# Kernel optimization log

Measured on AMD Instinct MI355X. Metric: run time of the kernel, lower is better.

The kernel has to match this reference:

```python
import jax, jax.numpy as jnp
import numpy as np

N = 50000      # nodes
E = 800000     # edges
D = 64         # out_feats
L = 5          # n_steps


def setup_inputs() -> dict:
    key = jax.random.key(0)
    ks = jax.random.split(key, 6)
    x = jax.random.normal(ks[0], (N, D), dtype=jnp.float32)
    edge_index = jax.random.randint(ks[1], (2, E), 0, N, dtype=jnp.int64)
    # per-layer message transform weights, uniform(-1/sqrt(D), 1/sqrt(D)) like PyG `uniform`
    bound = 1.0 / np.sqrt(D)
    weight = jax.random.uniform(ks[2], (L, D, D), minval=-bound, maxval=bound, dtype=jnp.float32)
    # GRUCell params (PyTorch layout: [3*D, D] with gate order r, z, n)
    w_ih = jax.random.uniform(ks[3], (3 * D, D), minval=-bound, maxval=bound, dtype=jnp.float32)
    w_hh = jax.random.uniform(ks[4], (3 * D, D), minval=-bound, maxval=bound, dtype=jnp.float32)
    b = jax.random.uniform(ks[5], (2, 3 * D), minval=-bound, maxval=bound, dtype=jnp.float32)
    return {"x": x, "edge_index": edge_index, "weight": weight,
            "w_ih": w_ih, "w_hh": w_hh, "b_ih": b[0], "b_hh": b[1]}


def _gru_cell(m, h, w_ih, w_hh, b_ih, b_hh):
    # PyTorch GRUCell semantics; gate order r, z, n
    gi = m @ w_ih.T + b_ih          # [N, 3D]
    gh = h @ w_hh.T + b_hh          # [N, 3D]
    i_r, i_z, i_n = jnp.split(gi, 3, axis=-1)
    h_r, h_z, h_n = jnp.split(gh, 3, axis=-1)
    r = jax.nn.sigmoid(i_r + h_r)
    z = jax.nn.sigmoid(i_z + h_z)
    n = jnp.tanh(i_n + r * h_n)
    return (1.0 - z) * n + z * h


def reference(x, edge_index, weight, w_ih, w_hh, b_ih, b_hh):
    src, dst = edge_index[0], edge_index[1]  # messages flow src (j) -> dst (i)
    h = x  # input width == out_channels, so padding branch is a no-op
    for i in range(L):
        m = h @ weight[i]                                   # [N, D]
        agg = jax.ops.segment_sum(m[src], dst, num_segments=N)  # scatter-add over edges
        h = _gru_cell(agg, h, w_ih, w_hh, b_ih, b_hh)
    return h
```

## Files before the change

kernel.cpp:

```cpp
#include <hip/hip_runtime.h>
#include <hip/hip_bf16.h>
#include <math.h>

#define DF 64
#define NPB 128
#define EPB 2048
#define DCAP 4608

typedef __attribute__((ext_vector_type(8))) short short8v;
typedef __attribute__((ext_vector_type(4))) float f32x4;

__global__ __launch_bounds__(256) void zero_int_kernel(int* __restrict__ p, int n) {
  int i = blockIdx.x * 256 + threadIdx.x;
  if (i < n) p[i] = 0;
}

__global__ __launch_bounds__(256) void bkt_count_kernel(const int* __restrict__ dst,
                                                        int* __restrict__ bcount,
                                                        int e, int nbk) {
  __shared__ int cnt[512];
  for (int i = threadIdx.x; i < nbk; i += 256) cnt[i] = 0;
  __syncthreads();
  const int eb = blockIdx.x * EPB;
  const int ee = (eb + EPB < e) ? (eb + EPB) : e;
  for (int i = eb + threadIdx.x; i < ee; i += 256) atomicAdd(&cnt[dst[i] >> 7], 1);
  __syncthreads();
  for (int i = threadIdx.x; i < nbk; i += 256)
    if (cnt[i]) atomicAdd(&bcount[i], cnt[i]);
}

__global__ __launch_bounds__(512) void bkt_scan_kernel(const int* __restrict__ bcount,
                                                       int* __restrict__ boff,
                                                       int* __restrict__ bcur,
                                                       int* __restrict__ rowp_last,
                                                       int e, int nbk) {
  __shared__ int a[512];
  const int t = threadIdx.x;
  int v = (t < nbk) ? bcount[t] : 0;
  a[t] = v;
  __syncthreads();
  for (int off = 1; off < 512; off <<= 1) {
    int add = (t >= off) ? a[t - off] : 0;
    __syncthreads();
    a[t] += add;
    __syncthreads();
  }
  int excl = a[t] - v;
  if (t < nbk) { boff[t] = excl; bcur[t] = excl; }
  if (t == nbk - 1) { boff[nbk] = excl + v; rowp_last[0] = e; }
}

__global__ __launch_bounds__(256) void bkt_fill_kernel(const int* __restrict__ src,
                                                       const int* __restrict__ dst,
                                                       int* __restrict__ bcur,
                                                       int2* __restrict__ bpairs,
                                                       int e, int nbk) {
  __shared__ int cnt[512];
  __shared__ int base[512];
  for (int i = threadIdx.x; i < nbk; i += 256) cnt[i] = 0;
  __syncthreads();
  const int eb = blockIdx.x * EPB;
  int s[8], d[8], r[8];
#pragma unroll
  for (int q = 0; q < 8; ++q) {
    int i = eb + q * 256 + threadIdx.x;
    bool ok = i < e;
    s[q] = ok ? src[i] : 0;
    d[q] = ok ? dst[i] : 0;
    r[q] = ok ? atomicAdd(&cnt[d[q] >> 7], 1) : 0;
  }
  __syncthreads();
  for (int i = threadIdx.x; i < nbk; i += 256)
    base[i] = cnt[i] ? atomicAdd(&bcur[i], cnt[i]) : 0;
  __syncthreads();
#pragma unroll
  for (int q = 0; q < 8; ++q) {
    int i = eb + q * 256 + threadIdx.x;
    if (i < e) {
      int b = d[q] >> 7;
      bpairs[base[b] + r[q]] = make_int2(s[q], d[q] & (NPB - 1));
    }
  }
}

__global__ __launch_bounds__(256) void bkt_csr_kernel(const int2* __restrict__ bpairs,
                                                      const int* __restrict__ boff,
                                                      int* __restrict__ rowp,
                                                      int* __restrict__ csr,
                                                      int n, int nbk) {
  __shared__ int cnt[NPB], cur[NPB], sa[NPB];
  __shared__ int lsrc[DCAP], ldst[DCAP], lcsr[DCAP];
  const int b = blockIdx.x;
  const int t = threadIdx.x;
  const int e0 = boff[b];
  int cnt_e = boff[b + 1] - e0;
  if (cnt_e > DCAP) cnt_e = DCAP;
  if (t < NPB) cnt[t] = 0;
  __syncthreads();
  for (int i = t; i < cnt_e; i += 256) {
    int2 p = bpairs[e0 + i];
    lsrc[i] = p.x;
    ldst[i] = p.y;
    atomicAdd(&cnt[p.y], 1);
  }
  __syncthreads();
  if (t < NPB) sa[t] = cnt[t];
  __syncthreads();
  for (int off = 1; off < NPB; off <<= 1) {
    int add = (t < NPB && t >= off) ? sa[t - off] : 0;
    __syncthreads();
    if (t < NPB) sa[t] += add;
    __syncthreads();
  }
  if (t < NPB) {
    int excl = sa[t] - cnt[t];
    cur[t] = excl;
    int node = b * NPB + t;
    if (node < n) rowp[node] = e0 + excl;
  }
  __syncthreads();
  for (int i = t; i < cnt_e; i += 256) {
    int p = atomicAdd(&cur[ldst[i]], 1);
    lcsr[p] = lsrc[i];
  }
  __syncthreads();
  for (int i = t; i < cnt_e; i += 256) csr[e0 + i] = lcsr[i];
}

__global__ __launch_bounds__(256) void wb_kernel(const float* __restrict__ W,
                                                 const float* __restrict__ wih,
                                                 const float* __restrict__ whh,
                                                 __hip_bfloat16* __restrict__ WB,
                                                 int total) {
  int idx = blockIdx.x * 256 + threadIdx.x;
  if (idx >= total) return;
  int k = idx & 127;
  int c = (idx >> 7) & 255;
  int l = idx >> 15;
  int g = c >> 6;
  int f = c & 63;
  float v = 0.f;
  if (k < 64) {
    if (g != 3) {
      int crow = (g == 0) ? f : (g == 1) ? (64 + f) : (128 + f);
      const float* wr = W + ((size_t)l * 64 + k) * 64;
      const float* ir = wih + (size_t)crow * 64;
      float s = 0.f;
#pragma unroll
      for (int t2 = 0; t2 < 64; ++t2) s = fmaf(wr[t2], ir[t2], s);
      v = s;
    }
  } else {
    if (g != 2) {
      int crow = (g == 0) ? f : (g == 1) ? (64 + f) : (128 + f);
      v = whh[(size_t)crow * 64 + (k - 64)];
    }
  }
  WB[idx] = __float2bfloat16(v);
}

__global__ __launch_bounds__(256) void cvt_kernel(const float* __restrict__ x,
                                                  __hip_bfloat16* __restrict__ o, int n) {
  int i = blockIdx.x * 256 + threadIdx.x;
  if (i < n) o[i] = __float2bfloat16(x[i]);
}

__global__ __launch_bounds__(256) void gather_kernel(const __hip_bfloat16* __restrict__ hb,
                                                     const int* __restrict__ rowp,
                                                     const int* __restrict__ csr,
                                                     __hip_bfloat16* __restrict__ segHb,
                                                     int n) {
  int w = (int)((blockIdx.x * 256 + threadIdx.x) >> 6);
  if (w >= n) return;
  const int lane = threadIdx.x & 63;
  const int g = lane >> 4;
  const int fq = lane & 15;
  const int beg = rowp[w], end = rowp[w + 1];
  float a0 = 0.f, a1 = 0.f, a2 = 0.f, a3 = 0.f;
  int e = beg + g;
  for (; e + 4 < end; e += 8) {
    int s0 = csr[e], s1 = csr[e + 4];
    uint2 v0 = *(const uint2*)(hb + (size_t)s0 * DF + fq * 4);
    uint2 v1 = *(const uint2*)(hb + (size_t)s1 * DF + fq * 4);
    a0 += __uint_as_float(v0.x << 16);
    a1 += __uint_as_float(v0.x & 0xffff0000u);
    a2 += __uint_as_float(v0.y << 16);
    a3 += __uint_as_float(v0.y & 0xffff0000u);
    a0 += __uint_as_float(v1.x << 16);
    a1 += __uint_as_float(v1.x & 0xffff0000u);
    a2 += __uint_as_float(v1.y << 16);
    a3 += __uint_as_float(v1.y & 0xffff0000u);
  }
  if (e < end) {
    int s0 = csr[e];
    uint2 v0 = *(const uint2*)(hb + (size_t)s0 * DF + fq * 4);
    a0 += __uint_as_float(v0.x << 16);
    a1 += __uint_as_float(v0.x & 0xffff0000u);
    a2 += __uint_as_float(v0.y << 16);
    a3 += __uint_as_float(v0.y & 0xffff0000u);
  }
  a0 += __shfl_xor(a0, 16); a1 += __shfl_xor(a1, 16);
  a2 += __shfl_xor(a2, 16); a3 += __shfl_xor(a3, 16);
  a0 += __shfl_xor(a0, 32); a1 += __shfl_xor(a1, 32);
  a2 += __shfl_xor(a2, 32); a3 += __shfl_xor(a3, 32);
  if (g == 0) {
    ushort2 p0 = make_ushort2(__bfloat16_as_ushort(__float2bfloat16(a0)),
                              __bfloat16_as_ushort(__float2bfloat16(a1)));
    ushort2 p1 = make_ushort2(__bfloat16_as_ushort(__float2bfloat16(a2)),
                              __bfloat16_as_ushort(__float2bfloat16(a3)));
    uint2 packed = make_uint2(((uint)p0.y << 16) | p0.x, ((uint)p1.y << 16) | p1.x);
    *(uint2*)(segHb + (size_t)w * DF + fq * 4) = packed;
  }
}

__device__ __forceinline__ short8v ldB(const char* sB, int c, int chunk) {
  return *(const short8v*)(sB + c * 256 + ((chunk ^ (c & 15)) * 16));
}

#define MFMA(acc, a, b) acc = __builtin_amdgcn_mfma_f32_16x16x32_bf16(a, b, acc, 0, 0, 0)

__global__ __launch_bounds__(256, 2) void gru_mfma_kernel(
    const __hip_bfloat16* __restrict__ segHb,
    __hip_bfloat16* __restrict__ hbf,
    const float* __restrict__ bih, const float* __restrict__ bhh,
    const __hip_bfloat16* __restrict__ WB, float* __restrict__ out,
    int writeOut, int n) {
  __shared__ __hip_bfloat16 sB[256 * 128];
#pragma unroll
  for (int i = 0; i < 16; ++i) {
    int idx = i * 256 + threadIdx.x;
    int c = idx >> 4, ch = idx & 15;
    short8v v = *(const short8v*)(WB + (size_t)c * 128 + ch * 8);
    *(short8v*)((char*)sB + c * 256 + ((ch ^ (c & 15)) * 16)) = v;
  }
  __syncthreads();

  const char* sBc = (const char*)sB;
  const int lane = threadIdx.x & 63;
  const int wid = threadIdx.x >> 6;
  const int row = lane & 15;
  const int quad = lane >> 4;
  const int ch0 = quad, ch1 = 4 + quad, ch2 = 8 + quad, ch3 = 12 + quad;

  float bi_r[4], bi_z[4], bi_n[4], bh_r[4], bh_z[4], bh_n[4];
#pragma unroll
  for (int j = 0; j < 4; ++j) {
    int f = j * 16 + row;
    bi_r[j] = bih[f]; bi_z[j] = bih[64 + f]; bi_n[j] = bih[128 + f];
    bh_r[j] = bhh[f]; bh_z[j] = bhh[64 + f]; bh_n[j] = bhh[128 + f];
  }

  for (int nb0 = blockIdx.x * 64; nb0 < n; nb0 += gridDim.x * 64) {
    const int nb = nb0 + wid * 16;
    if (nb >= n) continue;
    const short8v a0 = *(const short8v*)(segHb + (size_t)(nb + row) * DF + quad * 8);
    const short8v a1 = *(const short8v*)(segHb + (size_t)(nb + row) * DF + 32 + quad * 8);
    const short8v a2 = *(const short8v*)(hbf + (size_t)(nb + row) * DF + quad * 8);
    const short8v a3 = *(const short8v*)(hbf + (size_t)(nb + row) * DF + 32 + quad * 8);

    f32x4 accR[4], accZ[4], accN[4], accH[4];
#pragma unroll
    for (int j = 0; j < 4; ++j) {
      accR[j] = (f32x4){0.f, 0.f, 0.f, 0.f};
      accZ[j] = (f32x4){0.f, 0.f, 0.f, 0.f};
      accN[j] = (f32x4){0.f, 0.f, 0.f, 0.f};
      accH[j] = (f32x4){0.f, 0.f, 0.f, 0.f};
    }
#pragma unroll
    for (int j = 0; j < 4; ++j) {
      MFMA(accR[j], a0, ldB(sBc, j * 16 + row, ch0));
      MFMA(accR[j], a1, ldB(sBc, j * 16 + row, ch1));
      MFMA(accR[j], a2, ldB(sBc, j * 16 + row, ch2));
      MFMA(accR[j], a3, ldB(sBc, j * 16 + row, ch3));
      MFMA(accZ[j], a0, ldB(sBc, 64 + j * 16 + row, ch0));
      MFMA(accZ[j], a1, ldB(sBc, 64 + j * 16 + row, ch1));
      MFMA(accZ[j], a2, ldB(sBc, 64 + j * 16 + row, ch2));
      MFMA(accZ[j], a3, ldB(sBc, 64 + j * 16 + row, ch3));
      MFMA(accN[j], a0, ldB(sBc, 128 + j * 16 + row, ch0));
      MFMA(accN[j], a1, ldB(sBc, 128 + j * 16 + row, ch1));
      MFMA(accH[j], a2, ldB(sBc, 192 + j * 16 + row, ch2));
      MFMA(accH[j], a3, ldB(sBc, 192 + j * 16 + row, ch3));
    }
#pragma unroll
    for (int j = 0; j < 4; ++j) {
#pragma unroll
      for (int e = 0; e < 4; ++e) {
        const int node = nb + quad * 4 + e;
        const int f = j * 16 + row;
        const float hprev = __bfloat162float(hbf[(size_t)node * DF + f]);
        const float r = 1.f / (1.f + __expf(-(accR[j][e] + bi_r[j] + bh_r[j])));
        const float z = 1.f / (1.f + __expf(-(accZ[j][e] + bi_z[j] + bh_z[j])));
        const float nn = tanhf(accN[j][e] + bi_n[j] + r * (accH[j][e] + bh_n[j]));
        const float ho = fmaf(z, hprev - nn, nn);
        hbf[(size_t)node * DF + f] = __float2bfloat16(ho);
        if (writeOut) out[(size_t)node * DF + f] = ho;
      }
    }
  }
}

extern "C" void kernel_launch(void* const* d_in, const int* in_sizes, int n_in,
                              void* d_out, int out_size, void* d_ws, size_t ws_size,
                              hipStream_t stream) {
  const float* x   = (const float*)d_in[0];
  const int*   ei  = (const int*)d_in[1];
  const float* wgt = (const float*)d_in[2];
  const float* wih = (const float*)d_in[3];
  const float* whh = (const float*)d_in[4];
  const float* bih = (const float*)d_in[5];
  const float* bhh = (const float*)d_in[6];
  float* out = (float*)d_out;

  const int N = in_sizes[0] / DF;
  const int E = in_sizes[1] / 2;
  const int L = in_sizes[2] / (DF * DF);

  const int* srcv = ei;
  const int* dstv = ei + E;

  __hip_bfloat16* segHb = (__hip_bfloat16*)d_ws;
  __hip_bfloat16* hbf   = segHb + (size_t)N * DF;
  __hip_bfloat16* WB    = hbf + (size_t)N * DF;
  int* rowp   = (int*)(WB + (size_t)L * 256 * 128);
  int* csr    = rowp + (N + 1);
  int* bcount = csr + E;
  int* boff   = bcount + 512;
  int* bcur   = boff + 513;
  int2* bpairs = (int2*)(bcur + 512);

  const int NBK = (N + NPB - 1) >> 7;
  const int EB  = (E + EPB - 1) / EPB;

  zero_int_kernel<<<(NBK + 255) / 256, 256, 0, stream>>>(bcount, NBK);
  bkt_count_kernel<<<EB, 256, 0, stream>>>(dstv, bcount, E, NBK);
  bkt_scan_kernel<<<1, 512, 0, stream>>>(bcount, boff, bcur, rowp + N, E, NBK);
  bkt_fill_kernel<<<EB, 256, 0, stream>>>(srcv, dstv, bcur, bpairs, E, NBK);
  bkt_csr_kernel<<<NBK, 256, 0, stream>>>(bpairs, boff, rowp, csr, N, NBK);

  wb_kernel<<<(L * 256 * 128 + 255) / 256, 256, 0, stream>>>(wgt, wih, whh, WB,
                                                             L * 256 * 128);
  cvt_kernel<<<(N * DF + 255) / 256, 256, 0, stream>>>(x, hbf, N * DF);

  const int gruGrid = (N + 63) / 64;
  for (int i = 0; i < L; ++i) {
    gather_kernel<<<(N * DF + 255) / 256, 256, 0, stream>>>(hbf, rowp, csr, segHb, N);
    gru_mfma_kernel<<<gruGrid, 256, 0, stream>>>(segHb, hbf, bih, bhh,
                                                 WB + (size_t)i * 256 * 128, out,
                                                 (i == L - 1) ? 1 : 0, N);
  }
}
```

Measured before the change: 337.9 us.

## Split hidden state into two feature halves and gather each half separately

Stores the bf16 hidden state and the aggregated messages as two separate 32-feature planes instead of one 64-feature row-major array. The gather now runs twice per step, once per half, with 8 lanes per edge and 8 edges in flight per wave, so each pass's working set (about 3.2 MB) fits better in cache during random source lookups. The GRU kernel reads and writes the two planes. The cost is an extra launch per step, reading the CSR indices twice, and 64-byte per-node rows that may use memory transactions less fully.

```diff
diff --git a/kernel.cpp b/kernel.cpp
--- a/kernel.cpp
+++ b/kernel.cpp
@@ -160,28 +160,31 @@
 }
 
 __global__ __launch_bounds__(256) void cvt_kernel(const float* __restrict__ x,
-                                                  __hip_bfloat16* __restrict__ o, int n) {
+                                                  __hip_bfloat16* __restrict__ hA,
+                                                  __hip_bfloat16* __restrict__ hB, int n) {
   int i = blockIdx.x * 256 + threadIdx.x;
-  if (i < n) o[i] = __float2bfloat16(x[i]);
-}
-
-__global__ __launch_bounds__(256) void gather_kernel(const __hip_bfloat16* __restrict__ hb,
-                                                     const int* __restrict__ rowp,
-                                                     const int* __restrict__ csr,
-                                                     __hip_bfloat16* __restrict__ segHb,
-                                                     int n) {
+  if (i >= n) return;
+  int f = i & 63, node = i >> 6;
+  __hip_bfloat16 v = __float2bfloat16(x[i]);
+  if (f < 32) hA[(size_t)node * 32 + f] = v;
+  else        hB[(size_t)node * 32 + (f - 32)] = v;
+}
+
+__global__ __launch_bounds__(256) void gather_half_kernel(
+    const __hip_bfloat16* __restrict__ hX, const int* __restrict__ rowp,
+    const int* __restrict__ csr, __hip_bfloat16* __restrict__ segX, int n) {
   int w = (int)((blockIdx.x * 256 + threadIdx.x) >> 6);
   if (w >= n) return;
   const int lane = threadIdx.x & 63;
-  const int g = lane >> 4;
-  const int fq = lane & 15;
+  const int g = lane >> 3;
+  const int fl = lane & 7;
   const int beg = rowp[w], end = rowp[w + 1];
   float a0 = 0.f, a1 = 0.f, a2 = 0.f, a3 = 0.f;
   int e = beg + g;
-  for (; e + 4 < end; e += 8) {
-    int s0 = csr[e], s1 = csr[e + 4];
-    uint2 v0 = *(const uint2*)(hb + (size_t)s0 * DF + fq * 4);
-    uint2 v1 = *(const uint2*)(hb + (size_t)s1 * DF + fq * 4);
+  for (; e + 8 < end; e += 16) {
+    int s0 = csr[e], s1 = csr[e + 8];
+    uint2 v0 = *(const uint2*)(hX + (size_t)s0 * 32 + fl * 4);
+    uint2 v1 = *(const uint2*)(hX + (size_t)s1 * 32 + fl * 4);
     a0 += __uint_as_float(v0.x << 16);
     a1 += __uint_as_float(v0.x & 0xffff0000u);
     a2 += __uint_as_float(v0.y << 16);
@@ -193,12 +196,14 @@
   }
   if (e < end) {
     int s0 = csr[e];
-    uint2 v0 = *(const uint2*)(hb + (size_t)s0 * DF + fq * 4);
+    uint2 v0 = *(const uint2*)(hX + (size_t)s0 * 32 + fl * 4);
     a0 += __uint_as_float(v0.x << 16);
     a1 += __uint_as_float(v0.x & 0xffff0000u);
     a2 += __uint_as_float(v0.y << 16);
     a3 += __uint_as_float(v0.y & 0xffff0000u);
   }
+  a0 += __shfl_xor(a0, 8);  a1 += __shfl_xor(a1, 8);
+  a2 += __shfl_xor(a2, 8);  a3 += __shfl_xor(a3, 8);
   a0 += __shfl_xor(a0, 16); a1 += __shfl_xor(a1, 16);
   a2 += __shfl_xor(a2, 16); a3 += __shfl_xor(a3, 16);
   a0 += __shfl_xor(a0, 32); a1 += __shfl_xor(a1, 32);
@@ -209,7 +214,7 @@
     ushort2 p1 = make_ushort2(__bfloat16_as_ushort(__float2bfloat16(a2)),
                               __bfloat16_as_ushort(__float2bfloat16(a3)));
     uint2 packed = make_uint2(((uint)p0.y << 16) | p0.x, ((uint)p1.y << 16) | p1.x);
-    *(uint2*)(segHb + (size_t)w * DF + fq * 4) = packed;
+    *(uint2*)(segX + (size_t)w * 32 + fl * 4) = packed;
   }
 }
 
@@ -220,8 +225,8 @@
 #define MFMA(acc, a, b) acc = __builtin_amdgcn_mfma_f32_16x16x32_bf16(a, b, acc, 0, 0, 0)
 
 __global__ __launch_bounds__(256, 2) void gru_mfma_kernel(
-    const __hip_bfloat16* __restrict__ segHb,
-    __hip_bfloat16* __restrict__ hbf,
+    const __hip_bfloat16* __restrict__ segA, const __hip_bfloat16* __restrict__ segB,
+    __hip_bfloat16* __restrict__ hA, __hip_bfloat16* __restrict__ hB,
     const float* __restrict__ bih, const float* __restrict__ bhh,
     const __hip_bfloat16* __restrict__ WB, float* __restrict__ out,
     int writeOut, int n) {
@@ -253,10 +258,11 @@
   for (int nb0 = blockIdx.x * 64; nb0 < n; nb0 += gridDim.x * 64) {
     const int nb = nb0 + wid * 16;
     if (nb >= n) continue;
-    const short8v a0 = *(const short8v*)(segHb + (size_t)(nb + row) * DF + quad * 8);
-    const short8v a1 = *(const short8v*)(segHb + (size_t)(nb + row) * DF + 32 + quad * 8);
-    const short8v a2 = *(const short8v*)(hbf + (size_t)(nb + row) * DF + quad * 8);
-    const short8v a3 = *(const short8v*)(hbf + (size_t)(nb + row) * DF + 32 + quad * 8);
+    const size_t ro = (size_t)(nb + row) * 32 + quad * 8;
+    const short8v a0 = *(const short8v*)(segA + ro);
+    const short8v a1 = *(const short8v*)(segB + ro);
+    const short8v a2 = *(const short8v*)(hA + ro);
+    const short8v a3 = *(const short8v*)(hB + ro);
 
     f32x4 accR[4], accZ[4], accN[4], accH[4];
 #pragma unroll
@@ -283,16 +289,18 @@
     }
 #pragma unroll
     for (int j = 0; j < 4; ++j) {
+      __hip_bfloat16* hX = (j < 2) ? hA : hB;
+      const int fo = ((j & 1) << 4) + row;
 #pragma unroll
       for (int e = 0; e < 4; ++e) {
         const int node = nb + quad * 4 + e;
         const int f = j * 16 + row;
-        const float hprev = __bfloat162float(hbf[(size_t)node * DF + f]);
+        const float hprev = __bfloat162float(hX[(size_t)node * 32 + fo]);
         const float r = 1.f / (1.f + __expf(-(accR[j][e] + bi_r[j] + bh_r[j])));
         const float z = 1.f / (1.f + __expf(-(accZ[j][e] + bi_z[j] + bh_z[j])));
         const float nn = tanhf(accN[j][e] + bi_n[j] + r * (accH[j][e] + bh_n[j]));
         const float ho = fmaf(z, hprev - nn, nn);
-        hbf[(size_t)node * DF + f] = __float2bfloat16(ho);
+        hX[(size_t)node * 32 + fo] = __float2bfloat16(ho);
         if (writeOut) out[(size_t)node * DF + f] = ho;
       }
     }
@@ -318,9 +326,11 @@
   const int* srcv = ei;
   const int* dstv = ei + E;
 
-  __hip_bfloat16* segHb = (__hip_bfloat16*)d_ws;
-  __hip_bfloat16* hbf   = segHb + (size_t)N * DF;
-  __hip_bfloat16* WB    = hbf + (size_t)N * DF;
+  __hip_bfloat16* hA   = (__hip_bfloat16*)d_ws;
+  __hip_bfloat16* hB   = hA + (size_t)N * 32;
+  __hip_bfloat16* segA = hB + (size_t)N * 32;
+  __hip_bfloat16* segB = segA + (size_t)N * 32;
+  __hip_bfloat16* WB   = segB + (size_t)N * 32;
   int* rowp   = (int*)(WB + (size_t)L * 256 * 128);
   int* csr    = rowp + (N + 1);
   int* bcount = csr + E;
@@ -339,12 +349,14 @@
 
   wb_kernel<<<(L * 256 * 128 + 255) / 256, 256, 0, stream>>>(wgt, wih, whh, WB,
                                                              L * 256 * 128);
-  cvt_kernel<<<(N * DF + 255) / 256, 256, 0, stream>>>(x, hbf, N * DF);
-
+  cvt_kernel<<<(N * DF + 255) / 256, 256, 0, stream>>>(x, hA, hB, N * DF);
+
+  const int gatherGrid = (N * DF + 255) / 256;
   const int gruGrid = (N + 63) / 64;
   for (int i = 0; i < L; ++i) {
-    gather_kernel<<<(N * DF + 255) / 256, 256, 0, stream>>>(hbf, rowp, csr, segHb, N);
-    gru_mfma_kernel<<<gruGrid, 256, 0, stream>>>(segHb, hbf, bih, bhh,
+    gather_half_kernel<<<gatherGrid, 256, 0, stream>>>(hA, rowp, csr, segA, N);
+    gather_half_kernel<<<gatherGrid, 256, 0, stream>>>(hB, rowp, csr, segB, N);
+    gru_mfma_kernel<<<gruGrid, 256, 0, stream>>>(segA, segB, hA, hB, bih, bhh,
                                                  WB + (size_t)i * 256 * 128, out,
                                                  (i == L - 1) ? 1 : 0, N);
   }
```

New measurement: 387.3 us. 1.15x slower.

## Fuse neighbor gather into GRU MFMA kernel with ping-pong hidden buffers

Applied to the files above, without the earlier changes.

Merges the per-layer CSR gather and the GRU MFMA kernel into one layer kernel. Each block first aggregates neighbor features for its 64 nodes into a swizzled shared-memory tile, then runs the MFMA GRU using that tile. Hidden state now ping-pongs between two bf16 buffers because other blocks read the previous layer's h while this block writes. This removes the segHb global round-trip and one launch per layer. In exchange the gather now uses 16 lanes per node with a shorter unroll, and the block does the gather and GRU phases in sequence, which may lower latency hiding.

```diff
diff --git a/kernel.cpp b/kernel.cpp
--- a/kernel.cpp
+++ b/kernel.cpp
@@ -165,67 +165,24 @@
   if (i < n) o[i] = __float2bfloat16(x[i]);
 }
 
-__global__ __launch_bounds__(256) void gather_kernel(const __hip_bfloat16* __restrict__ hb,
-                                                     const int* __restrict__ rowp,
-                                                     const int* __restrict__ csr,
-                                                     __hip_bfloat16* __restrict__ segHb,
-                                                     int n) {
-  int w = (int)((blockIdx.x * 256 + threadIdx.x) >> 6);
-  if (w >= n) return;
-  const int lane = threadIdx.x & 63;
-  const int g = lane >> 4;
-  const int fq = lane & 15;
-  const int beg = rowp[w], end = rowp[w + 1];
-  float a0 = 0.f, a1 = 0.f, a2 = 0.f, a3 = 0.f;
-  int e = beg + g;
-  for (; e + 4 < end; e += 8) {
-    int s0 = csr[e], s1 = csr[e + 4];
-    uint2 v0 = *(const uint2*)(hb + (size_t)s0 * DF + fq * 4);
-    uint2 v1 = *(const uint2*)(hb + (size_t)s1 * DF + fq * 4);
-    a0 += __uint_as_float(v0.x << 16);
-    a1 += __uint_as_float(v0.x & 0xffff0000u);
-    a2 += __uint_as_float(v0.y << 16);
-    a3 += __uint_as_float(v0.y & 0xffff0000u);
-    a0 += __uint_as_float(v1.x << 16);
-    a1 += __uint_as_float(v1.x & 0xffff0000u);
-    a2 += __uint_as_float(v1.y << 16);
-    a3 += __uint_as_float(v1.y & 0xffff0000u);
-  }
-  if (e < end) {
-    int s0 = csr[e];
-    uint2 v0 = *(const uint2*)(hb + (size_t)s0 * DF + fq * 4);
-    a0 += __uint_as_float(v0.x << 16);
-    a1 += __uint_as_float(v0.x & 0xffff0000u);
-    a2 += __uint_as_float(v0.y << 16);
-    a3 += __uint_as_float(v0.y & 0xffff0000u);
-  }
-  a0 += __shfl_xor(a0, 16); a1 += __shfl_xor(a1, 16);
-  a2 += __shfl_xor(a2, 16); a3 += __shfl_xor(a3, 16);
-  a0 += __shfl_xor(a0, 32); a1 += __shfl_xor(a1, 32);
-  a2 += __shfl_xor(a2, 32); a3 += __shfl_xor(a3, 32);
-  if (g == 0) {
-    ushort2 p0 = make_ushort2(__bfloat16_as_ushort(__float2bfloat16(a0)),
-                              __bfloat16_as_ushort(__float2bfloat16(a1)));
-    ushort2 p1 = make_ushort2(__bfloat16_as_ushort(__float2bfloat16(a2)),
-                              __bfloat16_as_ushort(__float2bfloat16(a3)));
-    uint2 packed = make_uint2(((uint)p0.y << 16) | p0.x, ((uint)p1.y << 16) | p1.x);
-    *(uint2*)(segHb + (size_t)w * DF + fq * 4) = packed;
-  }
-}
-
 __device__ __forceinline__ short8v ldB(const char* sB, int c, int chunk) {
   return *(const short8v*)(sB + c * 256 + ((chunk ^ (c & 15)) * 16));
 }
 
+__device__ __forceinline__ short8v ldSeg(const char* sS, int nl, int c) {
+  return *(const short8v*)(sS + nl * 128 + ((c ^ (nl & 7)) * 16));
+}
+
 #define MFMA(acc, a, b) acc = __builtin_amdgcn_mfma_f32_16x16x32_bf16(a, b, acc, 0, 0, 0)
 
-__global__ __launch_bounds__(256, 2) void gru_mfma_kernel(
-    const __hip_bfloat16* __restrict__ segHb,
-    __hip_bfloat16* __restrict__ hbf,
+__global__ __launch_bounds__(256, 2) void layer_kernel(
+    const __hip_bfloat16* __restrict__ hIn, __hip_bfloat16* __restrict__ hOut,
+    const int* __restrict__ rowp, const int* __restrict__ csr,
     const float* __restrict__ bih, const float* __restrict__ bhh,
     const __hip_bfloat16* __restrict__ WB, float* __restrict__ out,
     int writeOut, int n) {
   __shared__ __hip_bfloat16 sB[256 * 128];
+  __shared__ __hip_bfloat16 sSeg[64 * 64];
 #pragma unroll
   for (int i = 0; i < 16; ++i) {
     int idx = i * 256 + threadIdx.x;
@@ -233,14 +190,61 @@
     short8v v = *(const short8v*)(WB + (size_t)c * 128 + ch * 8);
     *(short8v*)((char*)sB + c * 256 + ((ch ^ (c & 15)) * 16)) = v;
   }
+
+  const int tile = blockIdx.x * 64;
+  {
+    const int g = threadIdx.x >> 4;
+    const int l16 = threadIdx.x & 15;
+#pragma unroll
+    for (int q = 0; q < 4; ++q) {
+      const int nl = g + q * 16;
+      const int node = tile + nl;
+      float a0 = 0.f, a1 = 0.f, a2 = 0.f, a3 = 0.f;
+      if (node < n) {
+        int e = rowp[node];
+        const int end = rowp[node + 1];
+        for (; e + 1 < end; e += 2) {
+          int s0 = csr[e], s1 = csr[e + 1];
+          uint2 v0 = *(const uint2*)(hIn + (size_t)s0 * DF + l16 * 4);
+          uint2 v1 = *(const uint2*)(hIn + (size_t)s1 * DF + l16 * 4);
+          a0 += __uint_as_float(v0.x << 16);
+          a1 += __uint_as_float(v0.x & 0xffff0000u);
+          a2 += __uint_as_float(v0.y << 16);
+          a3 += __uint_as_float(v0.y & 0xffff0000u);
+          a0 += __uint_as_float(v1.x << 16);
+          a1 += __uint_as_float(v1.x & 0xffff0000u);
+          a2 += __uint_as_float(v1.y << 16);
+          a3 += __uint_as_float(v1.y & 0xffff0000u);
+        }
+        if (e < end) {
+          int s0 = csr[e];
+          uint2 v0 = *(const uint2*)(hIn + (size_t)s0 * DF + l16 * 4);
+          a0 += __uint_as_float(v0.x << 16);
+          a1 += __uint_as_float(v0.x & 0xffff0000u);
+          a2 += __uint_as_float(v0.y << 16);
+          a3 += __uint_as_float(v0.y & 0xffff0000u);
+        }
+      }
+      ushort2 p0 = make_ushort2(__bfloat16_as_ushort(__float2bfloat16(a0)),
+                                __bfloat16_as_ushort(__float2bfloat16(a1)));
+      ushort2 p1 = make_ushort2(__bfloat16_as_ushort(__float2bfloat16(a2)),
+                                __bfloat16_as_ushort(__float2bfloat16(a3)));
+      uint2 packed = make_uint2(((uint)p0.y << 16) | p0.x, ((uint)p1.y << 16) | p1.x);
+      char* p = (char*)sSeg + nl * 128 + (((l16 >> 1) ^ (nl & 7)) * 16) + (l16 & 1) * 8;
+      *(uint2*)p = packed;
+    }
+  }
   __syncthreads();
 
   const char* sBc = (const char*)sB;
+  const char* sSc = (const char*)sSeg;
   const int lane = threadIdx.x & 63;
   const int wid = threadIdx.x >> 6;
   const int row = lane & 15;
   const int quad = lane >> 4;
   const int ch0 = quad, ch1 = 4 + quad, ch2 = 8 + quad, ch3 = 12 + quad;
+  const int nb = tile + wid * 16;
+  if (nb >= n) return;
 
   float bi_r[4], bi_z[4], bi_n[4], bh_r[4], bh_z[4], bh_n[4];
 #pragma unroll
@@ -250,51 +254,49 @@
     bh_r[j] = bhh[f]; bh_z[j] = bhh[64 + f]; bh_n[j] = bhh[128 + f];
   }
 
-  for (int nb0 = blockIdx.x * 64; nb0 < n; nb0 += gridDim.x * 64) {
-    const int nb = nb0 + wid * 16;
-    if (nb >= n) continue;
-    const short8v a0 = *(const short8v*)(segHb + (size_t)(nb + row) * DF + quad * 8);
-    const short8v a1 = *(const short8v*)(segHb + (size_t)(nb + row) * DF + 32 + quad * 8);
-    const short8v a2 = *(const short8v*)(hbf + (size_t)(nb + row) * DF + quad * 8);
-    const short8v a3 = *(const short8v*)(hbf + (size_t)(nb + row) * DF + 32 + quad * 8);
-
-    f32x4 accR[4], accZ[4], accN[4], accH[4];
-#pragma unroll
-    for (int j = 0; j < 4; ++j) {
-      accR[j] = (f32x4){0.f, 0.f, 0.f, 0.f};
-      accZ[j] = (f32x4){0.f, 0.f, 0.f, 0.f};
-      accN[j] = (f32x4){0.f, 0.f, 0.f, 0.f};
-      accH[j] = (f32x4){0.f, 0.f, 0.f, 0.f};
-    }
-#pragma unroll
-    for (int j = 0; j < 4; ++j) {
-      MFMA(accR[j], a0, ldB(sBc, j * 16 + row, ch0));
-      MFMA(accR[j], a1, ldB(sBc, j * 16 + row, ch1));
-      MFMA(accR[j], a2, ldB(sBc, j * 16 + row, ch2));
-      MFMA(accR[j], a3, ldB(sBc, j * 16 + row, ch3));
-      MFMA(accZ[j], a0, ldB(sBc, 64 + j * 16 + row, ch0));
-      MFMA(accZ[j], a1, ldB(sBc, 64 + j * 16 + row, ch1));
-      MFMA(accZ[j], a2, ldB(sBc, 64 + j * 16 + row, ch2));
-      MFMA(accZ[j], a3, ldB(sBc, 64 + j * 16 + row, ch3));
-      MFMA(accN[j], a0, ldB(sBc, 128 + j * 16 + row, ch0));
-      MFMA(accN[j], a1, ldB(sBc, 128 + j * 16 + row, ch1));
-      MFMA(accH[j], a2, ldB(sBc, 192 + j * 16 + row, ch2));
-      MFMA(accH[j], a3, ldB(sBc, 192 + j * 16 + row, ch3));
-    }
-#pragma unroll
-    for (int j = 0; j < 4; ++j) {
-#pragma unroll
-      for (int e = 0; e < 4; ++e) {
-        const int node = nb + quad * 4 + e;
-        const int f = j * 16 + row;
-        const float hprev = __bfloat162float(hbf[(size_t)node * DF + f]);
-        const float r = 1.f / (1.f + __expf(-(accR[j][e] + bi_r[j] + bh_r[j])));
-        const float z = 1.f / (1.f + __expf(-(accZ[j][e] + bi_z[j] + bh_z[j])));
-        const float nn = tanhf(accN[j][e] + bi_n[j] + r * (accH[j][e] + bh_n[j]));
-        const float ho = fmaf(z, hprev - nn, nn);
-        hbf[(size_t)node * DF + f] = __float2bfloat16(ho);
-        if (writeOut) out[(size_t)node * DF + f] = ho;
-      }
+  const int nl = wid * 16 + row;
+  const short8v a0 = ldSeg(sSc, nl, quad);
+  const short8v a1 = ldSeg(sSc, nl, 4 + quad);
+  const short8v a2 = *(const short8v*)(hIn + (size_t)(nb + row) * DF + quad * 8);
+  const short8v a3 = *(const short8v*)(hIn + (size_t)(nb + row) * DF + 32 + quad * 8);
+
+  f32x4 accR[4], accZ[4], accN[4], accH[4];
+#pragma unroll
+  for (int j = 0; j < 4; ++j) {
+    accR[j] = (f32x4){0.f, 0.f, 0.f, 0.f};
+    accZ[j] = (f32x4){0.f, 0.f, 0.f, 0.f};
+    accN[j] = (f32x4){0.f, 0.f, 0.f, 0.f};
+    accH[j] = (f32x4){0.f, 0.f, 0.f, 0.f};
+  }
+#pragma unroll
+  for (int j = 0; j < 4; ++j) {
+    MFMA(accR[j], a0, ldB(sBc, j * 16 + row, ch0));
+    MFMA(accR[j], a1, ldB(sBc, j * 16 + row, ch1));
+    MFMA(accR[j], a2, ldB(sBc, j * 16 + row, ch2));
+    MFMA(accR[j], a3, ldB(sBc, j * 16 + row, ch3));
+    MFMA(accZ[j], a0, ldB(sBc, 64 + j * 16 + row, ch0));
+    MFMA(accZ[j], a1, ldB(sBc, 64 + j * 16 + row, ch1));
+    MFMA(accZ[j], a2, ldB(sBc, 64 + j * 16 + row, ch2));
+    MFMA(accZ[j], a3, ldB(sBc, 64 + j * 16 + row, ch3));
+    MFMA(accN[j], a0, ldB(sBc, 128 + j * 16 + row, ch0));
+    MFMA(accN[j], a1, ldB(sBc, 128 + j * 16 + row, ch1));
+    MFMA(accH[j], a2, ldB(sBc, 192 + j * 16 + row, ch2));
+    MFMA(accH[j], a3, ldB(sBc, 192 + j * 16 + row, ch3));
+  }
+#pragma unroll
+  for (int j = 0; j < 4; ++j) {
+#pragma unroll
+    for (int e = 0; e < 4; ++e) {
+      const int node = nb + quad * 4 + e;
+      if (node >= n) continue;
+      const int f = j * 16 + row;
+      const float hprev = __bfloat162float(hIn[(size_t)node * DF + f]);
+      const float r = 1.f / (1.f + __expf(-(accR[j][e] + bi_r[j] + bh_r[j])));
+      const float z = 1.f / (1.f + __expf(-(accZ[j][e] + bi_z[j] + bh_z[j])));
+      const float nn = tanhf(accN[j][e] + bi_n[j] + r * (accH[j][e] + bh_n[j]));
+      const float ho = fmaf(z, hprev - nn, nn);
+      if (writeOut) out[(size_t)node * DF + f] = ho;
+      else hOut[(size_t)node * DF + f] = __float2bfloat16(ho);
     }
   }
 }
@@ -318,9 +320,9 @@
   const int* srcv = ei;
   const int* dstv = ei + E;
 
-  __hip_bfloat16* segHb = (__hip_bfloat16*)d_ws;
-  __hip_bfloat16* hbf   = segHb + (size_t)N * DF;
-  __hip_bfloat16* WB    = hbf + (size_t)N * DF;
+  __hip_bfloat16* h0 = (__hip_bfloat16*)d_ws;
+  __hip_bfloat16* h1 = h0 + (size_t)N * DF;
+  __hip_bfloat16* WB = h1 + (size_t)N * DF;
   int* rowp   = (int*)(WB + (size_t)L * 256 * 128);
   int* csr    = rowp + (N + 1);
   int* bcount = csr + E;
@@ -339,13 +341,14 @@
 
   wb_kernel<<<(L * 256 * 128 + 255) / 256, 256, 0, stream>>>(wgt, wih, whh, WB,
                                                              L * 256 * 128);
-  cvt_kernel<<<(N * DF + 255) / 256, 256, 0, stream>>>(x, hbf, N * DF);
-
-  const int gruGrid = (N + 63) / 64;
+  cvt_kernel<<<(N * DF + 255) / 256, 256, 0, stream>>>(x, h0, N * DF);
+
+  const int grid = (N + 63) / 64;
   for (int i = 0; i < L; ++i) {
-    gather_kernel<<<(N * DF + 255) / 256, 256, 0, stream>>>(hbf, rowp, csr, segHb, N);
-    gru_mfma_kernel<<<gruGrid, 256, 0, stream>>>(segHb, hbf, bih, bhh,
-                                                 WB + (size_t)i * 256 * 128, out,
-                                                 (i == L - 1) ? 1 : 0, N);
-  }
-}
+    const __hip_bfloat16* hIn = (i & 1) ? h1 : h0;
+    __hip_bfloat16* hOut = (i & 1) ? h0 : h1;
+    layer_kernel<<<grid, 256, 0, stream>>>(hIn, hOut, rowp, csr, bih, bhh,
+                                           WB + (size_t)i * 256 * 128, out,
+                                           (i == L - 1) ? 1 : 0, N);
+  }
+}
```

Result: slower. 507.6 us (+50.2%).
